# Kernel optimization log

Hardware: AMD Instinct MI355X
Metric: run time of the kernel (lower is better)

Reference implementation:

```python
import jax, jax.numpy as jnp
import numpy as np

D_MODEL = 1024
N_HEADS = 16
D_K = D_MODEL // N_HEADS  # 64
B, T = 2, 2048


def setup_inputs() -> dict:
    key = jax.random.key(0)
    ks = jax.random.split(key, 6)
    s = 0.02
    x = jax.random.normal(ks[0], (B, T, D_MODEL), dtype=jnp.float32)
    # Stacked per-head projection weights, [H, C, d_k] (no bias, mini-gpt style)
    Wq = jax.random.normal(ks[1], (N_HEADS, D_MODEL, D_K), dtype=jnp.float32) * s
    Wk = jax.random.normal(ks[2], (N_HEADS, D_MODEL, D_K), dtype=jnp.float32) * s
    Wv = jax.random.normal(ks[3], (N_HEADS, D_MODEL, D_K), dtype=jnp.float32) * s
    # Output projection, torch nn.Linear(d_model, d_model): y = x @ Wo.T + bo
    Wo = jax.random.normal(ks[4], (D_MODEL, D_MODEL), dtype=jnp.float32) * s
    bo = jax.random.normal(ks[5], (D_MODEL,), dtype=jnp.float32) * s
    return {"x": x, "Wq": Wq, "Wk": Wk, "Wv": Wv, "Wo": Wo, "bo": bo}


def reference(x, Wq, Wk, Wv, Wo, bo):
    Bq, Tq, C = x.shape
    # Batched per-head projections (replaces the per-head Python loop)
    q = jnp.einsum('btc,hck->bhtk', x, Wq)  # [B,H,T,dk]
    k = jnp.einsum('btc,hck->bhtk', x, Wk)
    v = jnp.einsum('btc,hck->bhtk', x, Wv)
    scale = 1.0 / jnp.sqrt(jnp.asarray(D_K, dtype=x.dtype))
    scores = jnp.einsum('bhtk,bhsk->bhts', q, k) * scale  # [B,H,T,T]
    causal = jnp.tril(jnp.ones((Tq, Tq), dtype=bool))
    scores = jnp.where(causal, scores, jnp.asarray(-1e9, dtype=scores.dtype))
    attn = jax.nn.softmax(scores, axis=-1)
    out = jnp.einsum('bhts,bhsk->bhtk', attn, v)  # [B,H,T,dk]
    # concat heads -> [B,T,C]
    out = out.transpose(0, 2, 1, 3).reshape(Bq, Tq, C)
    return jnp.einsum('btc,dc->btd', out, Wo) + bo
```

## Files before the change

kernel.cpp:

```cpp
#include <hip/hip_runtime.h>
#include <hip/hip_bf16.h>


using short8 = __attribute__((ext_vector_type(8))) short;
using f32x4  = __attribute__((ext_vector_type(4))) float;
using fp16x2 = __attribute__((ext_vector_type(2))) __fp16;
using half4  = __attribute__((ext_vector_type(4))) _Float16;
using half8  = __attribute__((ext_vector_type(8))) _Float16;

#define SCALE_LOG2E 0.18033688011112042f

__device__ __forceinline__ unsigned short f2bf(float f) {
    union { float f; unsigned u; } v; v.f = f;
    unsigned r = v.u + 0x7fffu + ((v.u >> 16) & 1u);
    return (unsigned short)(r >> 16);
}

__device__ __forceinline__ void gld16(const unsigned short* gp, unsigned short* lp) {
    __builtin_amdgcn_global_load_lds(
        (const __attribute__((address_space(1))) void*)(gp),
        (__attribute__((address_space(3))) void*)(unsigned int)(unsigned long long)(lp),
        16, 0, 0);
}

__global__ void prep(const float* __restrict__ x,
                     const float* __restrict__ Wq,
                     const float* __restrict__ Wk,
                     const float* __restrict__ Wv,
                     const float* __restrict__ Wo,
                     unsigned short* __restrict__ xb,
                     unsigned short* __restrict__ wfrag,
                     unsigned short* __restrict__ wofrag) {
    __shared__ float tile[64][65];
    int blk = blockIdx.x;
    int t = threadIdx.x;
    if (blk < 768) {
        int b = blk;
        int cchunk = b & 15;
        int h = (b >> 4) & 15;
        int s = b >> 8;
        const float* W = (s == 0) ? Wq : ((s == 1) ? Wk : Wv);
        float sc = (s == 0) ? SCALE_LOG2E : 1.0f;
        const float* src = W + (h * 1024 + cchunk * 64) * 64;
        #pragma unroll
        for (int it = 0; it < 4; ++it) {
            int idx = (it * 256 + t) * 4;
            int cc = idx >> 6, kk = idx & 63;
            float4 v = *(const float4*)(src + idx);
            tile[cc][kk + 0] = v.x; tile[cc][kk + 1] = v.y;
            tile[cc][kk + 2] = v.z; tile[cc][kk + 3] = v.w;
        }
        __syncthreads();
        int sh = s * 16 + h;
        #pragma unroll
        for (int p = 0; p < 2; ++p) {
            int slot = p * 256 + t;
            int d   = slot & 63;
            int cc8 = slot >> 6;
            int n16  = sh * 4 + (d >> 4);
            int col  = d & 15;
            int kq   = cchunk * 2 + (cc8 >> 2);
            int quad = cc8 & 3;
            ushort4 lo, hi;
            lo.x = f2bf(tile[cc8 * 8 + 0][d] * sc); lo.y = f2bf(tile[cc8 * 8 + 1][d] * sc);
            lo.z = f2bf(tile[cc8 * 8 + 2][d] * sc); lo.w = f2bf(tile[cc8 * 8 + 3][d] * sc);
            hi.x = f2bf(tile[cc8 * 8 + 4][d] * sc); hi.y = f2bf(tile[cc8 * 8 + 5][d] * sc);
            hi.z = f2bf(tile[cc8 * 8 + 6][d] * sc); hi.w = f2bf(tile[cc8 * 8 + 7][d] * sc);
            unsigned short* dst = wfrag + ((size_t)((n16 * 32 + kq) * 64 + quad * 16 + col)) * 8;
            *(ushort4*)dst = lo;
            *(ushort4*)(dst + 4) = hi;
        }
    } else if (blk < 1280) {
        int g = (blk - 768) * 256 + t;
        int col  = g & 15;
        int quad = (g >> 4) & 3;
        int kq   = (g >> 6) & 31;
        int n16  = g >> 11;
        const float* src = Wo + (size_t)(n16 * 16 + col) * 1024 + kq * 32 + quad * 8;
        float4 a = *(const float4*)src;
        float4 b2 = *(const float4*)(src + 4);
        ushort4 lo, hi;
        lo.x = f2bf(a.x); lo.y = f2bf(a.y); lo.z = f2bf(a.z); lo.w = f2bf(a.w);
        hi.x = f2bf(b2.x); hi.y = f2bf(b2.y); hi.z = f2bf(b2.z); hi.w = f2bf(b2.w);
        *(ushort4*)(wofrag + (size_t)g * 8)     = lo;
        *(ushort4*)(wofrag + (size_t)g * 8 + 4) = hi;
    } else {
        int i = (blk - 1280) * 256 + t;
        if (i < 1048576) {
            float4 v = ((const float4*)x)[i];
            ushort4 o;
            o.x = f2bf(v.x); o.y = f2bf(v.y); o.z = f2bf(v.z); o.w = f2bf(v.w);
            ((ushort4*)xb)[i] = o;
        }
    }
}

__global__ __launch_bounds__(256, 3) void qkv_gemm(
        const unsigned short* __restrict__ xb,
        const unsigned short* __restrict__ wtf,
        unsigned short* __restrict__ qB,
        unsigned short* __restrict__ kfrag,
        _Float16* __restrict__ vfrag) {
    __shared__ unsigned short Als[128 * 64];
    int wave = threadIdx.x >> 6;
    int lane = threadIdx.x & 63;
    int col  = lane & 15;
    int quad = lane >> 4;
    int l8r = lane >> 3;
    int l8c = lane & 7;
    int gkc = (l8c ^ l8r) * 8;
    int mq = wave >> 1;
    int nq = wave & 1;
    int m0 = blockIdx.x * 128;
    int n0 = blockIdx.y * 128 + nq * 64;
    int n16b = n0 >> 4;
    f32x4 acc[4][4] = {};
    for (int k0 = 0; k0 < 1024; k0 += 64) {
        int kq = k0 >> 5;
        __syncthreads();
        short8 bf0[4], bf1[4];
        #pragma unroll
        for (int nb = 0; nb < 4; ++nb) {
            bf0[nb] = *(const short8*)(wtf +
                ((size_t)((n16b + nb) * 32 + kq) * 64 + lane) * 8);
            bf1[nb] = *(const short8*)(wtf +
                ((size_t)((n16b + nb) * 32 + kq + 1) * 64 + lane) * 8);
        }
        #pragma unroll
        for (int j = 0; j < 4; ++j) {
            int row = wave * 32 + j * 8;
            gld16(xb + (size_t)(m0 + row + l8r) * 1024 + k0 + gkc, Als + row * 64);
        }
        __syncthreads();
        short8 af[4];
        #pragma unroll
        for (int i = 0; i < 4; ++i)
            af[i] = *(const short8*)(Als + (mq * 64 + i * 16 + col) * 64 +
                                     ((quad ^ (col & 7)) * 8));
        #pragma unroll
        for (int mb = 0; mb < 4; ++mb)
            #pragma unroll
            for (int nb = 0; nb < 4; ++nb)
                acc[mb][nb] = __builtin_amdgcn_mfma_f32_16x16x32_bf16(
                    af[mb], bf0[nb], acc[mb][nb], 0, 0, 0);
        #pragma unroll
        for (int i = 0; i < 4; ++i)
            af[i] = *(const short8*)(Als + (mq * 64 + i * 16 + col) * 64 +
                                     (((quad + 4) ^ (col & 7)) * 8));
        #pragma unroll
        for (int mb = 0; mb < 4; ++mb)
            #pragma unroll
            for (int nb = 0; nb < 4; ++nb)
                acc[mb][nb] = __builtin_amdgcn_mfma_f32_16x16x32_bf16(
                    af[mb], bf1[nb], acc[mb][nb], 0, 0, 0);
    }
    int wm0 = m0 + mq * 64;
    int sel = blockIdx.y >> 3;
    #pragma unroll
    for (int nb = 0; nb < 4; ++nb) {
        int n = n0 + nb * 16 + col;
        int d10 = n & 1023;
        int h_ = d10 >> 6, d = d10 & 63;
        if (sel == 0) {
            #pragma unroll
            for (int mb = 0; mb < 4; ++mb)
                #pragma unroll
                for (int r = 0; r < 4; ++r) {
                    int m = wm0 + mb * 16 + quad * 4 + r;
                    int b_ = m >> 11, t_ = m & 2047;
                    qB[((size_t)(b_ * 16 + h_) * 2048 + t_) * 64 + d] =
                        f2bf(acc[mb][nb][r]);
                }
        } else if (sel == 1) {
            int hK = d >> 5, quadk = (d >> 3) & 3, j = d & 7;
            #pragma unroll
            for (int mb = 0; mb < 4; ++mb)
                #pragma unroll
                for (int r = 0; r < 4; ++r) {
                    int m = wm0 + mb * 16 + quad * 4 + r;
                    int b_ = m >> 11, t_ = m & 2047;
                    int bh = b_ * 16 + h_;
                    kfrag[((((size_t)bh * 128 + (t_ >> 4)) * 2 + hK) * 64 +
                           quadk * 16 + (t_ & 15)) * 8 + j] = f2bf(acc[mb][nb][r]);
                }
        } else {
            int nbv = d >> 4, colv = d & 15;
            #pragma unroll
            for (int mb = 0; mb < 4; ++mb) {
                int m = wm0 + mb * 16 + quad * 4;
                int b_ = m >> 11, t_ = m & 2047;
                int bh = b_ * 16 + h_;
                half4 hv;
                hv[0] = (_Float16)acc[mb][nb][0]; hv[1] = (_Float16)acc[mb][nb][1];
                hv[2] = (_Float16)acc[mb][nb][2]; hv[3] = (_Float16)acc[mb][nb][3];
                *(half4*)(vfrag + ((((size_t)bh * 64 + (t_ >> 5)) * 4 + nbv) * 64 +
                          ((t_ >> 2) & 3) * 16 + colv) * 8 + ((t_ >> 4) & 1) * 4) = hv;
            }
        }
    }
}

__global__ __launch_bounds__(256, 4) void oproj(
        const unsigned short* __restrict__ A,
        const unsigned short* __restrict__ wof,
        const float* __restrict__ bo,
        float* __restrict__ y) {
    __shared__ unsigned short Als[64 * 64];
    int wave = threadIdx.x >> 6;
    int lane = threadIdx.x & 63;
    int col  = lane & 15;
    int quad = lane >> 4;
    int l8r = lane >> 3;
    int l8c = lane & 7;
    int gkc = (l8c ^ l8r) * 8;
    int mq = wave >> 1;
    int nq = wave & 1;
    int m0 = blockIdx.x * 64;
    int n0 = blockIdx.y * 128 + nq * 64;
    int n16b = n0 >> 4;
    f32x4 acc[2][4] = {};
    for (int k0 = 0; k0 < 1024; k0 += 64) {
        int kq = k0 >> 5;
        __syncthreads();
        short8 bf0[4], bf1[4];
        #pragma unroll
        for (int nb = 0; nb < 4; ++nb) {
            bf0[nb] = *(const short8*)(wof +
                ((size_t)((n16b + nb) * 32 + kq) * 64 + lane) * 8);
            bf1[nb] = *(const short8*)(wof +
                ((size_t)((n16b + nb) * 32 + kq + 1) * 64 + lane) * 8);
        }
        #pragma unroll
        for (int j = 0; j < 2; ++j) {
            int row = wave * 16 + j * 8;
            gld16(A + (size_t)(m0 + row + l8r) * 1024 + k0 + gkc, Als + row * 64);
        }
        __syncthreads();
        short8 af[2];
        #pragma unroll
        for (int i = 0; i < 2; ++i)
            af[i] = *(const short8*)(Als + (mq * 32 + i * 16 + col) * 64 +
                                     ((quad ^ (col & 7)) * 8));
        #pragma unroll
        for (int mb = 0; mb < 2; ++mb)
            #pragma unroll
            for (int nb = 0; nb < 4; ++nb)
                acc[mb][nb] = __builtin_amdgcn_mfma_f32_16x16x32_bf16(
                    af[mb], bf0[nb], acc[mb][nb], 0, 0, 0);
        #pragma unroll
        for (int i = 0; i < 2; ++i)
            af[i] = *(const short8*)(Als + (mq * 32 + i * 16 + col) * 64 +
                                     (((quad + 4) ^ (col & 7)) * 8));
        #pragma unroll
        for (int mb = 0; mb < 2; ++mb)
            #pragma unroll
            for (int nb = 0; nb < 4; ++nb)
                acc[mb][nb] = __builtin_amdgcn_mfma_f32_16x16x32_bf16(
                    af[mb], bf1[nb], acc[mb][nb], 0, 0, 0);
    }
    #pragma unroll
    for (int nb = 0; nb < 4; ++nb) {
        int n = n0 + nb * 16 + col;
        float bias = bo[n];
        #pragma unroll
        for (int mb = 0; mb < 2; ++mb)
            #pragma unroll
            for (int r = 0; r < 4; ++r) {
                int m = m0 + mq * 32 + mb * 16 + quad * 4 + r;
                y[(size_t)m * 1024 + n] = acc[mb][nb][r] + bias;
            }
    }
}

__global__ __launch_bounds__(256, 3) void attn(
        const unsigned short* __restrict__ qB,
        const unsigned short* __restrict__ kfrag,
        const _Float16* __restrict__ vfrag,
        unsigned short* __restrict__ aout) {
    __shared__ float O_comb[2][64][33];
    __shared__ float L_comb[2][2][2][16];
    int wave = threadIdx.x >> 6;
    int lane = threadIdx.x & 63;
    int col  = lane & 15;
    int quad = lane >> 4;
    int sl     = wave >> 1;
    int parity = wave & 1;
    int bh   = blockIdx.x & 31;
    int r    = blockIdx.x >> 8;
    int o    = (blockIdx.x >> 5) & 7;
    int pairidx = 31 - 8 * r - ((r & 1) ? (7 - o) : o);
    int strip = pairidx * 2 + sl;
    int q0 = strip * 32;
    const unsigned short* q = qB + (size_t)bh * 2048 * 64;
    const unsigned short* kf_base = kfrag + (size_t)bh * 128 * 2 * 512;
    const _Float16*       vf_base = vfrag + (size_t)bh * 64 * 4 * 512;

    short8 qf[2][2];
    #pragma unroll
    for (int qb = 0; qb < 2; ++qb)
        #pragma unroll
        for (int h = 0; h < 2; ++h)
            qf[qb][h] = *(const short8*)(q + (size_t)(q0 + qb * 16 + col) * 64 + h * 32 + quad * 8);

    f32x4 o_acc[2][4] = {};
    float l[2] = {0.f, 0.f};

    struct KV { short8 kf[2][2]; half8 vv[4]; };
    KV bufA, bufB;

    auto load_half = [&](int it, int kv32, KV& b) {
        int K16 = it * 4 + kv32 * 2;
        #pragma unroll
        for (int p = 0; p < 2; ++p)
            #pragma unroll
            for (int h = 0; h < 2; ++h)
                b.kf[p][h] = *(const short8*)(kf_base +
                    (((size_t)(K16 + p) * 2 + h) * 64 + lane) * 8);
        #pragma unroll
        for (int nb = 0; nb < 4; ++nb)
            b.vv[nb] = *(const half8*)(vf_base +
                (((size_t)(it * 2 + kv32) * 4 + nb) * 64 + lane) * 8);
    };

    auto compute_half = [&](int it, int kv32, KV& b) {
        int kv0 = it * 64;
        bool diag = (kv0 + 63 > q0);
        __builtin_amdgcn_s_setprio(1);
        #pragma unroll
        for (int par = 0; par < 2; ++par) {
            int kvbase = kv0 + kv32 * 32 + par * 16;
            f32x4 st[2] = {};
            #pragma unroll
            for (int qb = 0; qb < 2; ++qb) {
                st[qb] = __builtin_amdgcn_mfma_f32_16x16x32_bf16(b.kf[par][0], qf[qb][0], st[qb], 0, 0, 0);
                st[qb] = __builtin_amdgcn_mfma_f32_16x16x32_bf16(b.kf[par][1], qf[qb][1], st[qb], 0, 0, 0);
            }
            #pragma unroll
            for (int qb = 0; qb < 2; ++qb) {
                float p0 = __builtin_amdgcn_exp2f(st[qb][0]);
                float p1 = __builtin_amdgcn_exp2f(st[qb][1]);
                float p2 = __builtin_amdgcn_exp2f(st[qb][2]);
                float p3 = __builtin_amdgcn_exp2f(st[qb][3]);
                if (diag) {
                    int qg  = q0 + qb * 16 + col;
                    int kvg = kvbase + quad * 4;
                    p0 = (kvg + 0 > qg) ? 0.f : p0;
                    p1 = (kvg + 1 > qg) ? 0.f : p1;
                    p2 = (kvg + 2 > qg) ? 0.f : p2;
                    p3 = (kvg + 3 > qg) ? 0.f : p3;
                }
                l[qb] += (p0 + p1) + (p2 + p3);
                union { fp16x2 h2[2]; half4 h4; } cvt;
                cvt.h2[0] = __builtin_amdgcn_cvt_pkrtz(p0, p1);
                cvt.h2[1] = __builtin_amdgcn_cvt_pkrtz(p2, p3);
                half4 pf = cvt.h4;
                #pragma unroll
                for (int nb = 0; nb < 4; ++nb) {
                    half4 vf = (par == 0)
                        ? __builtin_shufflevector(b.vv[nb], b.vv[nb], 0, 1, 2, 3)
                        : __builtin_shufflevector(b.vv[nb], b.vv[nb], 4, 5, 6, 7);
                    o_acc[qb][nb] = __builtin_amdgcn_mfma_f32_16x16x16f16(pf, vf, o_acc[qb][nb], 0, 0, 0);
                }
            }
        }
        __builtin_amdgcn_s_setprio(0);
    };

    int n_iter = (q0 + 95) >> 6;
    if (parity < n_iter) load_half(parity, 0, bufA);
    for (int it = parity; it < n_iter; it += 2) {
        load_half(it, 1, bufB);
        compute_half(it, 0, bufA);
        if (it + 2 < n_iter) load_half(it + 2, 0, bufA);
        compute_half(it, 1, bufB);
    }

    #pragma unroll
    for (int qb = 0; qb < 2; ++qb) {
        float lr = l[qb];
        lr += __shfl_xor(lr, 16);
        lr += __shfl_xor(lr, 32);
        l[qb] = lr;
    }
    if (quad == 0) {
        L_comb[sl][parity][0][col] = l[0];
        L_comb[sl][parity][1][col] = l[1];
    }
    if (parity == 1) {
        #pragma unroll
        for (int qb = 0; qb < 2; ++qb)
            #pragma unroll
            for (int nb = 0; nb < 4; ++nb)
                #pragma unroll
                for (int rr = 0; rr < 4; ++rr)
                    O_comb[sl][lane][qb * 16 + nb * 4 + rr] = o_acc[qb][nb][rr];
    }
    __syncthreads();
    if (parity == 0) {
        int b_ = bh >> 4, h_ = bh & 15;
        #pragma unroll
        for (int qb = 0; qb < 2; ++qb)
            #pragma unroll
            for (int rr = 0; rr < 4; ++rr) {
                int qi = quad * 4 + rr;
                float inv_l = 1.0f / (L_comb[sl][0][qb][qi] + L_comb[sl][1][qb][qi]);
                int t_ = q0 + qb * 16 + qi;
                #pragma unroll
                for (int nb = 0; nb < 4; ++nb) {
                    float ov = o_acc[qb][nb][rr] + O_comb[sl][lane][qb * 16 + nb * 4 + rr];
                    aout[(size_t)(b_ * 2048 + t_) * 1024 + h_ * 64 + nb * 16 + col] =
                        f2bf(ov * inv_l);
                }
            }
    }
}

extern "C" void kernel_launch(void* const* d_in, const int* in_sizes, int n_in,
                              void* d_out, int out_size, void* d_ws, size_t ws_size,
                              hipStream_t stream) {
    const float* x  = (const float*)d_in[0];
    const float* Wq = (const float*)d_in[1];
    const float* Wk = (const float*)d_in[2];
    const float* Wv = (const float*)d_in[3];
    const float* Wo = (const float*)d_in[4];
    const float* bo = (const float*)d_in[5];
    float* y = (float*)d_out;

    unsigned short* xb    = (unsigned short*)d_ws;
    unsigned short* Wtf   = xb    + 4194304;
    unsigned short* Wof   = Wtf   + 3145728;
    unsigned short* qBb   = Wof   + 1048576;
    unsigned short* kfr   = qBb   + 4194304;
    unsigned short* vfr   = kfr   + 4194304;
    unsigned short* aout  = vfr   + 4194304;

    prep<<<5376, 256, 0, stream>>>(x, Wq, Wk, Wv, Wo, xb, Wtf, Wof);
    qkv_gemm<<<dim3(32, 24), 256, 0, stream>>>(xb, Wtf, qBb, kfr, (_Float16*)vfr);
    attn<<<1024, 256, 0, stream>>>(qBb, kfr, (const _Float16*)vfr, aout);
    oproj<<<dim3(64, 8), 256, 0, stream>>>(aout, Wof, bo, y);
}
```

Baseline: 164.8 us.

## Double-buffer LDS A tiles in QKV GEMM and simplify attention block ordering

The QKV projection GEMM now keeps two LDS buffers for the activation tile. It issues the asynchronous global-to-LDS load for the next K-slice while running MFMAs on the current one, which removes one barrier per iteration and hides load latency. The attention kernel's block-to-strip mapping drops the serpentine interleave in favour of a plain descending order of query-strip pairs. This doubles the GEMM's LDS footprint, which could limit occupancy, and changes how the causal attention work is balanced across CUs.

```diff
diff --git a/kernel.cpp b/kernel.cpp
--- a/kernel.cpp
+++ b/kernel.cpp
@@ -101,7 +101,7 @@
         unsigned short* __restrict__ qB,
         unsigned short* __restrict__ kfrag,
         _Float16* __restrict__ vfrag) {
-    __shared__ unsigned short Als[128 * 64];
+    __shared__ unsigned short Als[2][128 * 64];
     int wave = threadIdx.x >> 6;
     int lane = threadIdx.x & 63;
     int col  = lane & 15;
@@ -115,45 +115,61 @@
     int n0 = blockIdx.y * 128 + nq * 64;
     int n16b = n0 >> 4;
     f32x4 acc[4][4] = {};
-    for (int k0 = 0; k0 < 1024; k0 += 64) {
-        int kq = k0 >> 5;
-        __syncthreads();
-        short8 bf0[4], bf1[4];
-        #pragma unroll
-        for (int nb = 0; nb < 4; ++nb) {
-            bf0[nb] = *(const short8*)(wtf +
-                ((size_t)((n16b + nb) * 32 + kq) * 64 + lane) * 8);
-            bf1[nb] = *(const short8*)(wtf +
-                ((size_t)((n16b + nb) * 32 + kq + 1) * 64 + lane) * 8);
-        }
+
+    auto stage = [&](unsigned short* buf, int k0) {
         #pragma unroll
         for (int j = 0; j < 4; ++j) {
             int row = wave * 32 + j * 8;
-            gld16(xb + (size_t)(m0 + row + l8r) * 1024 + k0 + gkc, Als + row * 64);
-        }
-        __syncthreads();
+            gld16(xb + (size_t)(m0 + row + l8r) * 1024 + k0 + gkc, buf + row * 64);
+        }
+    };
+    auto loadB = [&](int kq, short8 (&b0)[4], short8 (&b1)[4]) {
+        #pragma unroll
+        for (int nb = 0; nb < 4; ++nb) {
+            b0[nb] = *(const short8*)(wtf +
+                ((size_t)((n16b + nb) * 32 + kq) * 64 + lane) * 8);
+            b1[nb] = *(const short8*)(wtf +
+                ((size_t)((n16b + nb) * 32 + kq + 1) * 64 + lane) * 8);
+        }
+    };
+    auto compute = [&](const unsigned short* ls, short8 (&b0)[4], short8 (&b1)[4]) {
         short8 af[4];
         #pragma unroll
         for (int i = 0; i < 4; ++i)
-            af[i] = *(const short8*)(Als + (mq * 64 + i * 16 + col) * 64 +
+            af[i] = *(const short8*)(ls + (mq * 64 + i * 16 + col) * 64 +
                                      ((quad ^ (col & 7)) * 8));
         #pragma unroll
         for (int mb = 0; mb < 4; ++mb)
             #pragma unroll
             for (int nb = 0; nb < 4; ++nb)
                 acc[mb][nb] = __builtin_amdgcn_mfma_f32_16x16x32_bf16(
-                    af[mb], bf0[nb], acc[mb][nb], 0, 0, 0);
+                    af[mb], b0[nb], acc[mb][nb], 0, 0, 0);
         #pragma unroll
         for (int i = 0; i < 4; ++i)
-            af[i] = *(const short8*)(Als + (mq * 64 + i * 16 + col) * 64 +
+            af[i] = *(const short8*)(ls + (mq * 64 + i * 16 + col) * 64 +
                                      (((quad + 4) ^ (col & 7)) * 8));
         #pragma unroll
         for (int mb = 0; mb < 4; ++mb)
             #pragma unroll
             for (int nb = 0; nb < 4; ++nb)
                 acc[mb][nb] = __builtin_amdgcn_mfma_f32_16x16x32_bf16(
-                    af[mb], bf1[nb], acc[mb][nb], 0, 0, 0);
-    }
+                    af[mb], b1[nb], acc[mb][nb], 0, 0, 0);
+    };
+
+    short8 bf0[4], bf1[4];
+    stage(Als[0], 0);
+    __syncthreads();
+    for (int t = 0; t < 16; t += 2) {
+        loadB(2 * t, bf0, bf1);
+        stage(Als[1], (t + 1) * 64);
+        compute(Als[0], bf0, bf1);
+        __syncthreads();
+        loadB(2 * t + 2, bf0, bf1);
+        if (t + 2 < 16) stage(Als[0], (t + 2) * 64);
+        compute(Als[1], bf0, bf1);
+        __syncthreads();
+    }
+
     int wm0 = m0 + mq * 64;
     int sel = blockIdx.y >> 3;
     #pragma unroll
@@ -286,9 +302,7 @@
     int sl     = wave >> 1;
     int parity = wave & 1;
     int bh   = blockIdx.x & 31;
-    int r    = blockIdx.x >> 8;
-    int o    = (blockIdx.x >> 5) & 7;
-    int pairidx = 31 - 8 * r - ((r & 1) ? (7 - o) : o);
+    int pairidx = 31 - (blockIdx.x >> 5);
     int strip = pairidx * 2 + sl;
     int q0 = strip * 32;
     const unsigned short* q = qB + (size_t)bh * 2048 * 64;
```

Result: no change. 162.8 us (-1.2%).
